# Kernel optimization log

Hardware: AMD Instinct MI355X
Metric: run time of the kernel (lower is better)

## Reference

```python
import jax, jax.numpy as jnp
import numpy as np

B_, N, C = 4096, 49, 384
H = 12
HD = C // H
NW = 64
SCALE = HD ** -0.5


def setup_inputs() -> dict:
    key = jax.random.key(0)
    k_x, k_m, k_w1, k_b1, k_w2, k_b2 = jax.random.split(key, 6)
    x = jax.random.normal(k_x, (B_, N, C), dtype=jnp.float32)
    # shifted-window style additive mask: 0 = allowed, -100 = blocked
    mask = jnp.where(jax.random.uniform(k_m, (NW, N, N)) < 0.5, 0.0, -100.0).astype(jnp.float32)
    w_qkv = jax.random.normal(k_w1, (3 * C, C), dtype=jnp.float32) * (C ** -0.5)
    b_qkv = jax.random.normal(k_b1, (3 * C,), dtype=jnp.float32) * 0.02
    w_proj = jax.random.normal(k_w2, (C, C), dtype=jnp.float32) * (C ** -0.5)
    b_proj = jax.random.normal(k_b2, (C,), dtype=jnp.float32) * 0.02
    return {"x": x, "mask": mask, "w_qkv": w_qkv, "b_qkv": b_qkv,
            "w_proj": w_proj, "b_proj": b_proj}


def reference(x, mask, w_qkv, b_qkv, w_proj, b_proj):
    # qkv projection: (B_, N, 3C)
    qkv = x @ w_qkv.T + b_qkv
    qkv = qkv.reshape(B_, N, 3, H, HD).transpose(2, 0, 3, 1, 4)  # (3, B_, H, N, HD)
    q, k, v = qkv[0], qkv[1], qkv[2]
    q = q * SCALE
    attn = jnp.einsum('bhnd,bhmd->bhnm', q, k)  # (B_, H, N, N)
    # additive shifted-window mask, per-window pattern broadcast over batch & heads
    attn = attn.reshape(B_ // NW, NW, H, N, N) + mask[None, :, None]
    attn = attn.reshape(B_, H, N, N)
    attn = jax.nn.softmax(attn, axis=-1)
    out = jnp.einsum('bhnm,bhmd->bhnd', attn, v)  # (B_, H, N, HD)
    out = out.transpose(0, 2, 1, 3).reshape(B_, N, C)
    return out @ w_proj.T + b_proj
```

## Files before the change

kernel.cpp:

```cpp
#include <hip/hip_runtime.h>
#include <cstdio>
#include <cstdint>


typedef __attribute__((ext_vector_type(8))) short bfrag8;
typedef __attribute__((ext_vector_type(4))) float facc4;
typedef __attribute__((ext_vector_type(16))) float facc16;

#define SCALE_Q 0.17677669529663687f
#define PLANE 6422528ull

__device__ __forceinline__ unsigned short f2bf(float f) {
  unsigned int x = __float_as_uint(f);
  x += 0x7fffu + ((x >> 16) & 1u);
  return (unsigned short)(x >> 16);
}

__device__ __forceinline__ void gload_lds16(const void* g, void* l) {
  __builtin_amdgcn_global_load_lds(
      (const __attribute__((address_space(1))) unsigned int*)g,
      (__attribute__((address_space(3))) unsigned int*)l,
      16, 0, 0);
}

__global__ void __launch_bounds__(256) prep_kernel(
    const float* __restrict__ wq, const float* __restrict__ wp,
    const float* __restrict__ mask,
    unsigned short* __restrict__ Bfq, unsigned short* __restrict__ Bfp,
    unsigned long long* __restrict__ bits) {
  const int blk = blockIdx.x;
  if (blk < 288) {
    const float* w = (blk < 216) ? wq : wp;
    unsigned short* Bf = (blk < 216) ? Bfq : Bfp;
    const int t = ((blk < 216) ? blk : blk - 216) * 256 + threadIdx.x;
    const int fid = t >> 6, lc = t & 63;
    const int cg = fid / 24, ksl = fid - cg * 24;
    const int col = cg * 32 + (lc & 31);
    const int k = ksl * 16 + (lc >> 5) * 8;
    const float* src = w + (size_t)col * 384 + k;
    unsigned short* dst = Bf + ((size_t)fid << 9) + (lc << 3);
#pragma unroll
    for (int j = 0; j < 8; ++j) dst[j] = f2bf(src[j]);
  } else {
    const int idx = (blk - 288) * 256 + threadIdx.x;
    const int wdw = idx >> 6, m = idx & 63;
    unsigned long long bm = 0ull;
    if (m < 49) {
      const float* mp = mask + (size_t)wdw * 2401 + (size_t)m * 49;
      for (int n = 0; n < 49; ++n)
        if (mp[n] > -50.f) bm |= (1ull << n);
    }
    bits[idx] = bm;
  }
}

#define LB32(dst, ks_)                                                         \
  {                                                                            \
    _Pragma("unroll") for (int ni = 0; ni < 3; ++ni)                           \
        dst[ni] = *(const bfrag8*)(                                            \
            Bf + ((size_t)((cg0 + ni) * 24 + (ks_)) << 9) + (lane << 3));      \
  }

#define MF32(bb, ks_)                                                          \
  {                                                                            \
    const bfrag8 af0 = *(const bfrag8*)(Ab + ((size_t)(ks_) << 10));           \
    const bfrag8 af1 = *(const bfrag8*)(Ab + ((size_t)(24 + (ks_)) << 10));    \
    _Pragma("unroll") for (int ni = 0; ni < 3; ++ni) {                         \
      acc[0][ni] = __builtin_amdgcn_mfma_f32_32x32x16_bf16(af0, bb[ni],        \
                                                           acc[0][ni], 0, 0, 0);\
      acc[1][ni] = __builtin_amdgcn_mfma_f32_32x32x16_bf16(af1, bb[ni],        \
                                                           acc[1][ni], 0, 0, 0);\
    }                                                                          \
  }

template <int NR, int MODE, int SWZ>
__global__ void __launch_bounds__(512, 1) gemm_32(
    const float* __restrict__ Af32, const unsigned short* __restrict__ Abf,
    const unsigned short* __restrict__ Bf, const float* __restrict__ bias,
    unsigned short* __restrict__ qkv, float* __restrict__ f_out) {
  __shared__ __align__(16) unsigned short Alds[128 * 384];

  int bid = blockIdx.x;
  bid = (bid & 7) * SWZ + (bid >> 3);
  const int tid = threadIdx.x;
  const int lane = tid & 63, w = tid >> 6;
  const int wr = w >> 2, wc = w & 3;
  const int l31 = lane & 31, l5 = lane >> 5;
  const size_t a_row0 = (size_t)bid * 128;

  if (MODE == 0) {
#pragma unroll
    for (int j = 0; j < 12; ++j) {
      const int fid = w + j * 8;
      const int rg = fid / 24, ksl = fid - rg * 24;
      const int row = rg * 32 + l31;
      const int k = ksl * 16 + l5 * 8;
      const float* src = Af32 + (a_row0 + row) * 384 + k;
      const float4 v0 = *(const float4*)(src);
      const float4 v1 = *(const float4*)(src + 4);
      bfrag8 h;
      h[0] = (short)f2bf(v0.x); h[1] = (short)f2bf(v0.y);
      h[2] = (short)f2bf(v0.z); h[3] = (short)f2bf(v0.w);
      h[4] = (short)f2bf(v1.x); h[5] = (short)f2bf(v1.y);
      h[6] = (short)f2bf(v1.z); h[7] = (short)f2bf(v1.w);
      *(bfrag8*)((char*)Alds + ((w << 10) + (j << 13)) + (lane << 4)) = h;
    }
  } else {
#pragma unroll
    for (int j = 0; j < 12; ++j) {
      const int fid = w + j * 8;
      const int rg = fid / 24, ksl = fid - rg * 24;
      const int row = rg * 32 + l31;
      const int k = ksl * 16 + l5 * 8;
      gload_lds16(Abf + (a_row0 + row) * 384 + k,
                  (char*)Alds + ((w << 10) + (j << 13)));
    }
  }
  __syncthreads();

  const char* Ab = (const char*)Alds + ((size_t)(wr * 48) << 10) + (lane << 4);

  for (int rnd = 0; rnd < NR; ++rnd) {
    const int cg0 = (rnd * 4 + wc) * 3;
    facc16 acc[2][3];
#pragma unroll
    for (int mi = 0; mi < 2; ++mi)
#pragma unroll
      for (int ni = 0; ni < 3; ++ni)
#pragma unroll
        for (int r = 0; r < 16; ++r) acc[mi][ni][r] = 0.f;

    bfrag8 bA[3], bB[3], bC[3];
    LB32(bA, 0);
    LB32(bB, 1);
    LB32(bC, 2);
#pragma unroll 1
    for (int ks = 0; ks < 24; ks += 3) {
      MF32(bA, ks);
      if (ks + 3 < 24) LB32(bA, ks + 3);
      MF32(bB, ks + 1);
      if (ks + 4 < 24) LB32(bB, ks + 4);
      MF32(bC, ks + 2);
      if (ks + 5 < 24) LB32(bC, ks + 5);
    }

    if (MODE == 0) {
#pragma unroll
      for (int ni = 0; ni < 3; ++ni) {
        const int j0 = (cg0 + ni) * 32;
        const int t = j0 / 384;
        const int rj = j0 - t * 384;
        const int h = rj >> 5;
        unsigned short* pl = qkv + (size_t)(t * 12 + h) * PLANE + l31;
        const float bvv = bias[j0 + l31];
        const float sc = (t == 0) ? SCALE_Q : 1.0f;
#pragma unroll
        for (int mi = 0; mi < 2; ++mi)
#pragma unroll
          for (int r = 0; r < 16; ++r) {
            const size_t m = a_row0 + wr * 64 + mi * 32 +
                             (r & 3) + 8 * (r >> 2) + 4 * l5;
            pl[m * 32] = f2bf((acc[mi][ni][r] + bvv) * sc);
          }
      }
    } else {
#pragma unroll
      for (int ni = 0; ni < 3; ++ni) {
        const int col = (cg0 + ni) * 32 + l31;
        const float bvv = bias[col];
#pragma unroll
        for (int mi = 0; mi < 2; ++mi)
#pragma unroll
          for (int r = 0; r < 16; ++r) {
            const size_t m = a_row0 + wr * 64 + mi * 32 +
                             (r & 3) + 8 * (r >> 2) + 4 * l5;
            f_out[m * 384 + col] = acc[mi][ni][r] + bvv;
          }
      }
    }
  }
}

__global__ void __launch_bounds__(64) attn_kernel(
    const unsigned short* __restrict__ QKV,
    const unsigned long long* __restrict__ mbits,
    unsigned short* __restrict__ Og) {
  __shared__ unsigned short Vt[32 * 64];
  __shared__ unsigned short Ps[64 * 64];

  const int bid = blockIdx.x;
  const int b = bid / 12, h = bid - b * 12;
  const int lane = threadIdx.x;
  const int l15 = lane & 15, l4 = lane >> 4;

  const bfrag8 z8 = {0, 0, 0, 0, 0, 0, 0, 0};
  const facc4 fz = {0.f, 0.f, 0.f, 0.f};

  const size_t wb = (size_t)b * 49 * 32;
  const unsigned short* Qp = QKV + (size_t)h * PLANE + wb;
  const unsigned short* Kp = QKV + (size_t)(12 + h) * PLANE + wb;
  const unsigned short* Vp = QKV + (size_t)(24 + h) * PLANE + wb;

#pragma unroll
  for (int i = 0; i < 4; ++i)
    *(bfrag8*)((char*)Vt + (lane + i * 64) * 16) = z8;

#pragma unroll
  for (int i = 0; i < 4; ++i) {
    const int c = lane + i * 64;
    if (c < 196) {
      const bfrag8 vv = *(const bfrag8*)(Vp + c * 8);
      const int n = c >> 2, cc = c & 3;
      const int d0 = cc * 8;
#pragma unroll
      for (int jj = 0; jj < 8; ++jj) {
        const int d = d0 + jj;
        *(unsigned short*)((char*)Vt + (((d << 7) + (n << 1)) ^ ((d & 7) << 4))) =
            (unsigned short)vv[jj];
      }
    }
  }
  __syncthreads();

  facc4 s[4][4];
  {
    bfrag8 qa[4], kf[4];
#pragma unroll
    for (int mi = 0; mi < 4; ++mi)
      qa[mi] = *(const bfrag8*)((const char*)Qp + (mi * 16 + l15) * 64 + l4 * 16);
#pragma unroll
    for (int ni = 0; ni < 4; ++ni)
      kf[ni] = *(const bfrag8*)((const char*)Kp + (ni * 16 + l15) * 64 + l4 * 16);
#pragma unroll
    for (int mi = 0; mi < 4; ++mi)
#pragma unroll
      for (int ni = 0; ni < 4; ++ni)
        s[mi][ni] = __builtin_amdgcn_mfma_f32_16x16x32_bf16(qa[mi], kf[ni], fz, 0, 0, 0);
  }

  const unsigned long long* mb = mbits + (size_t)(b & 63) * 64;
  float rinv[4][4];
#pragma unroll
  for (int mi = 0; mi < 4; ++mi)
#pragma unroll
    for (int r = 0; r < 4; ++r) {
      const int m = mi * 16 + l4 * 4 + r;
      const unsigned long long mw = mb[m];
      float mx = -1e30f;
      int ok[4];
#pragma unroll
      for (int ni = 0; ni < 4; ++ni) {
        const int n = ni * 16 + l15;
        ok[ni] = (int)((mw >> n) & 1ull);
        const float v = ok[ni] ? s[mi][ni][r] : -1e30f;
        mx = fmaxf(mx, v);
      }
      mx = fmaxf(mx, __shfl_xor(mx, 1));
      mx = fmaxf(mx, __shfl_xor(mx, 2));
      mx = fmaxf(mx, __shfl_xor(mx, 4));
      mx = fmaxf(mx, __shfl_xor(mx, 8));
      float sum = 0.f;
#pragma unroll
      for (int ni = 0; ni < 4; ++ni) {
        const float p = ok[ni] ? __expf(s[mi][ni][r] - mx) : 0.f;
        s[mi][ni][r] = p;
        sum += p;
      }
      sum += __shfl_xor(sum, 1);
      sum += __shfl_xor(sum, 2);
      sum += __shfl_xor(sum, 4);
      sum += __shfl_xor(sum, 8);
      rinv[mi][r] = 1.0f / sum;
#pragma unroll
      for (int ni = 0; ni < 4; ++ni) {
        const int n = ni * 16 + l15;
        *(unsigned short*)((char*)Ps + (((m << 7) + (n << 1)) ^ ((m & 7) << 4))) =
            f2bf(s[mi][ni][r]);
      }
    }
  __syncthreads();

  facc4 o[4][2];
#pragma unroll
  for (int mi = 0; mi < 4; ++mi)
#pragma unroll
    for (int di = 0; di < 2; ++di) o[mi][di] = fz;
#pragma unroll
  for (int kk = 0; kk < 2; ++kk) {
    bfrag8 pa[4], vb[2];
#pragma unroll
    for (int mi = 0; mi < 4; ++mi) {
      const int row = mi * 16 + l15;
      pa[mi] = *(const bfrag8*)((const char*)Ps +
                                (((row << 7) + kk * 64 + (l4 << 4)) ^ ((row & 7) << 4)));
    }
#pragma unroll
    for (int di = 0; di < 2; ++di) {
      const int row = di * 16 + l15;
      vb[di] = *(const bfrag8*)((const char*)Vt +
                                (((row << 7) + kk * 64 + (l4 << 4)) ^ ((row & 7) << 4)));
    }
#pragma unroll
    for (int mi = 0; mi < 4; ++mi)
#pragma unroll
      for (int di = 0; di < 2; ++di)
        o[mi][di] = __builtin_amdgcn_mfma_f32_16x16x32_bf16(pa[mi], vb[di], o[mi][di], 0, 0, 0);
  }

  unsigned short* op = Og + (size_t)b * 18816 + h * 32;
#pragma unroll
  for (int mi = 0; mi < 4; ++mi)
#pragma unroll
    for (int r = 0; r < 4; ++r) {
      const int m = mi * 16 + l4 * 4 + r;
      if (m < 49) {
        const float rs = rinv[mi][r];
#pragma unroll
        for (int di = 0; di < 2; ++di)
          op[(size_t)m * 384 + di * 16 + l15] = f2bf(o[mi][di][r] * rs);
      }
    }
}

extern "C" void kernel_launch(void* const* d_in, const int* in_sizes, int n_in,
                              void* d_out, int out_size, void* d_ws, size_t ws_size,
                              hipStream_t stream) {
  const float* x      = (const float*)d_in[0];
  const float* mask   = (const float*)d_in[1];
  const float* w_qkv  = (const float*)d_in[2];
  const float* b_qkv  = (const float*)d_in[3];
  const float* w_proj = (const float*)d_in[4];
  const float* b_proj = (const float*)d_in[5];
  float* out = (float*)d_out;

  const size_t E = 77070336ull;
  unsigned short* wsu   = (unsigned short*)d_ws;
  unsigned short* qkvp  = wsu;
  unsigned short* o_ws  = wsu + 3 * E;
  unsigned short* Bfq   = wsu + 4 * E;
  unsigned short* Bfp   = Bfq + 442368ull;
  unsigned long long* mb = (unsigned long long*)(Bfp + 147456ull);
  const size_t need = (4 * E + 442368ull + 147456ull) * 2ull + 4096ull * 8ull;
  if (ws_size < need) {
    fprintf(stderr, "[WindowAttention] ws too small: need=%zu have=%zu\n",
            (size_t)need, ws_size);
    return;
  }

  prep_kernel<<<304, 256, 0, stream>>>(w_qkv, w_proj, mask, Bfq, Bfp, mb);

  gemm_32<3, 0, 196><<<1568, 512, 0, stream>>>(x, nullptr, Bfq, b_qkv,
                                               qkvp, nullptr);

  attn_kernel<<<49152, 64, 0, stream>>>(qkvp, mb, o_ws);

  gemm_32<1, 1, 196><<<1568, 512, 0, stream>>>(nullptr, o_ws, Bfp, b_proj,
                                               nullptr, out);
}
```

Measured before the change: 650.5 us.

## Add weight-stationary projection GEMM and shorten QKV GEMM B prefetch depth

Adds a new output-projection GEMM kernel that stages half of the projection weight matrix (192 columns) in LDS per pass and streams the bf16 attention output rows directly from global memory into registers, instead of staging the activation tile in LDS. The QKV GEMM loses its MODE template and its B-fragment prefetch drops from three register buffers to two, which lowers register pressure but hides less load latency. The projection kernel now reloads weights twice per block and fetches the A operand from global memory inside the inner loop, so its performance depends on cache hit rates for those reads.

```diff
diff --git a/kernel.cpp b/kernel.cpp
--- a/kernel.cpp
+++ b/kernel.cpp
@@ -73,11 +73,10 @@
     }                                                                          \
   }
 
-template <int NR, int MODE, int SWZ>
+template <int NR, int SWZ>
 __global__ void __launch_bounds__(512, 1) gemm_32(
-    const float* __restrict__ Af32, const unsigned short* __restrict__ Abf,
-    const unsigned short* __restrict__ Bf, const float* __restrict__ bias,
-    unsigned short* __restrict__ qkv, float* __restrict__ f_out) {
+    const float* __restrict__ Af32, const unsigned short* __restrict__ Bf,
+    const float* __restrict__ bias, unsigned short* __restrict__ qkv) {
   __shared__ __align__(16) unsigned short Alds[128 * 384];
 
   int bid = blockIdx.x;
@@ -88,33 +87,21 @@
   const int l31 = lane & 31, l5 = lane >> 5;
   const size_t a_row0 = (size_t)bid * 128;
 
-  if (MODE == 0) {
-#pragma unroll
-    for (int j = 0; j < 12; ++j) {
-      const int fid = w + j * 8;
-      const int rg = fid / 24, ksl = fid - rg * 24;
-      const int row = rg * 32 + l31;
-      const int k = ksl * 16 + l5 * 8;
-      const float* src = Af32 + (a_row0 + row) * 384 + k;
-      const float4 v0 = *(const float4*)(src);
-      const float4 v1 = *(const float4*)(src + 4);
-      bfrag8 h;
-      h[0] = (short)f2bf(v0.x); h[1] = (short)f2bf(v0.y);
-      h[2] = (short)f2bf(v0.z); h[3] = (short)f2bf(v0.w);
-      h[4] = (short)f2bf(v1.x); h[5] = (short)f2bf(v1.y);
-      h[6] = (short)f2bf(v1.z); h[7] = (short)f2bf(v1.w);
-      *(bfrag8*)((char*)Alds + ((w << 10) + (j << 13)) + (lane << 4)) = h;
-    }
-  } else {
-#pragma unroll
-    for (int j = 0; j < 12; ++j) {
-      const int fid = w + j * 8;
-      const int rg = fid / 24, ksl = fid - rg * 24;
-      const int row = rg * 32 + l31;
-      const int k = ksl * 16 + l5 * 8;
-      gload_lds16(Abf + (a_row0 + row) * 384 + k,
-                  (char*)Alds + ((w << 10) + (j << 13)));
-    }
+#pragma unroll
+  for (int j = 0; j < 12; ++j) {
+    const int fid = w + j * 8;
+    const int rg = fid / 24, ksl = fid - rg * 24;
+    const int row = rg * 32 + l31;
+    const int k = ksl * 16 + l5 * 8;
+    const float* src = Af32 + (a_row0 + row) * 384 + k;
+    const float4 v0 = *(const float4*)(src);
+    const float4 v1 = *(const float4*)(src + 4);
+    bfrag8 h;
+    h[0] = (short)f2bf(v0.x); h[1] = (short)f2bf(v0.y);
+    h[2] = (short)f2bf(v0.z); h[3] = (short)f2bf(v0.w);
+    h[4] = (short)f2bf(v1.x); h[5] = (short)f2bf(v1.y);
+    h[6] = (short)f2bf(v1.z); h[7] = (short)f2bf(v1.w);
+    *(bfrag8*)((char*)Alds + ((w << 10) + (j << 13)) + (lane << 4)) = h;
   }
   __syncthreads();
 
@@ -130,54 +117,99 @@
 #pragma unroll
         for (int r = 0; r < 16; ++r) acc[mi][ni][r] = 0.f;
 
-    bfrag8 bA[3], bB[3], bC[3];
+    bfrag8 bA[3], bB[3];
     LB32(bA, 0);
     LB32(bB, 1);
-    LB32(bC, 2);
 #pragma unroll 1
-    for (int ks = 0; ks < 24; ks += 3) {
+    for (int ks = 0; ks < 24; ks += 2) {
       MF32(bA, ks);
-      if (ks + 3 < 24) LB32(bA, ks + 3);
+      if (ks + 2 < 24) LB32(bA, ks + 2);
       MF32(bB, ks + 1);
-      if (ks + 4 < 24) LB32(bB, ks + 4);
-      MF32(bC, ks + 2);
-      if (ks + 5 < 24) LB32(bC, ks + 5);
-    }
-
-    if (MODE == 0) {
-#pragma unroll
-      for (int ni = 0; ni < 3; ++ni) {
-        const int j0 = (cg0 + ni) * 32;
-        const int t = j0 / 384;
-        const int rj = j0 - t * 384;
-        const int h = rj >> 5;
-        unsigned short* pl = qkv + (size_t)(t * 12 + h) * PLANE + l31;
-        const float bvv = bias[j0 + l31];
-        const float sc = (t == 0) ? SCALE_Q : 1.0f;
-#pragma unroll
-        for (int mi = 0; mi < 2; ++mi)
-#pragma unroll
-          for (int r = 0; r < 16; ++r) {
-            const size_t m = a_row0 + wr * 64 + mi * 32 +
-                             (r & 3) + 8 * (r >> 2) + 4 * l5;
-            pl[m * 32] = f2bf((acc[mi][ni][r] + bvv) * sc);
-          }
-      }
-    } else {
-#pragma unroll
-      for (int ni = 0; ni < 3; ++ni) {
-        const int col = (cg0 + ni) * 32 + l31;
-        const float bvv = bias[col];
-#pragma unroll
-        for (int mi = 0; mi < 2; ++mi)
-#pragma unroll
-          for (int r = 0; r < 16; ++r) {
-            const size_t m = a_row0 + wr * 64 + mi * 32 +
-                             (r & 3) + 8 * (r >> 2) + 4 * l5;
-            f_out[m * 384 + col] = acc[mi][ni][r] + bvv;
-          }
-      }
-    }
+      if (ks + 3 < 24) LB32(bB, ks + 3);
+    }
+
+#pragma unroll
+    for (int ni = 0; ni < 3; ++ni) {
+      const int j0 = (cg0 + ni) * 32;
+      const int t = j0 / 384;
+      const int rj = j0 - t * 384;
+      const int h = rj >> 5;
+      unsigned short* pl = qkv + (size_t)(t * 12 + h) * PLANE + l31;
+      const float bvv = bias[j0 + l31];
+      const float sc = (t == 0) ? SCALE_Q : 1.0f;
+#pragma unroll
+      for (int mi = 0; mi < 2; ++mi)
+#pragma unroll
+        for (int r = 0; r < 16; ++r) {
+          const size_t m = a_row0 + wr * 64 + mi * 32 +
+                           (r & 3) + 8 * (r >> 2) + 4 * l5;
+          pl[m * 32] = f2bf((acc[mi][ni][r] + bvv) * sc);
+        }
+    }
+  }
+}
+
+template <int SWZ>
+__global__ void __launch_bounds__(512, 1) gemm_wp(
+    const unsigned short* __restrict__ O, const unsigned short* __restrict__ Bfp,
+    const float* __restrict__ bias, float* __restrict__ out) {
+  __shared__ __align__(16) unsigned short Wlds[144 * 512];
+
+  int bid = blockIdx.x;
+  bid = (bid & 7) * SWZ + (bid >> 3);
+  const int tid = threadIdx.x;
+  const int lane = tid & 63, w = tid >> 6;
+  const int wr = w >> 1, wc = w & 1;
+  const int l31 = lane & 31, l5 = lane >> 5;
+  const size_t a_row0 = (size_t)bid * 128;
+
+  const unsigned short* Orow = O + (a_row0 + wr * 32 + l31) * 384 + l5 * 8;
+  const char* Wb = (const char*)Wlds + ((size_t)(wc * 72) << 10) + (lane << 4);
+
+  for (int nh = 0; nh < 2; ++nh) {
+#pragma unroll
+    for (int j = 0; j < 18; ++j) {
+      const int fidl = w + j * 8;
+      gload_lds16(Bfp + ((size_t)(nh * 144 + fidl) << 9) + (lane << 3),
+                  (char*)Wlds + ((w << 10) + (j << 13)));
+    }
+    __syncthreads();
+
+    facc16 acc[3];
+#pragma unroll
+    for (int ni = 0; ni < 3; ++ni)
+#pragma unroll
+      for (int r = 0; r < 16; ++r) acc[ni][r] = 0.f;
+
+    bfrag8 oA = *(const bfrag8*)(Orow);
+    bfrag8 oB = *(const bfrag8*)(Orow + 16);
+#pragma unroll 1
+    for (int ks = 0; ks < 24; ks += 2) {
+#pragma unroll
+      for (int ni = 0; ni < 3; ++ni)
+        acc[ni] = __builtin_amdgcn_mfma_f32_32x32x16_bf16(
+            oA, *(const bfrag8*)(Wb + ((size_t)(ni * 24 + ks) << 10)),
+            acc[ni], 0, 0, 0);
+      if (ks + 2 < 24) oA = *(const bfrag8*)(Orow + (ks + 2) * 16);
+#pragma unroll
+      for (int ni = 0; ni < 3; ++ni)
+        acc[ni] = __builtin_amdgcn_mfma_f32_32x32x16_bf16(
+            oB, *(const bfrag8*)(Wb + ((size_t)(ni * 24 + ks + 1) << 10)),
+            acc[ni], 0, 0, 0);
+      if (ks + 3 < 24) oB = *(const bfrag8*)(Orow + (ks + 3) * 16);
+    }
+
+#pragma unroll
+    for (int ni = 0; ni < 3; ++ni) {
+      const int col = nh * 192 + (wc * 3 + ni) * 32 + l31;
+      const float bvv = bias[col];
+#pragma unroll
+      for (int r = 0; r < 16; ++r) {
+        const size_t m = a_row0 + wr * 32 + (r & 3) + 8 * (r >> 2) + 4 * l5;
+        out[m * 384 + col] = acc[ni][r] + bvv;
+      }
+    }
+    __syncthreads();
   }
 }
 
@@ -349,11 +381,9 @@
 
   prep_kernel<<<304, 256, 0, stream>>>(w_qkv, w_proj, mask, Bfq, Bfp, mb);
 
-  gemm_32<3, 0, 196><<<1568, 512, 0, stream>>>(x, nullptr, Bfq, b_qkv,
-                                               qkvp, nullptr);
+  gemm_32<3, 196><<<1568, 512, 0, stream>>>(x, Bfq, b_qkv, qkvp);
 
   attn_kernel<<<49152, 64, 0, stream>>>(qkvp, mb, o_ws);
 
-  gemm_32<1, 1, 196><<<1568, 512, 0, stream>>>(nullptr, o_ws, Bfp, b_proj,
-                                               nullptr, out);
-}
+  gemm_wp<196><<<1568, 512, 0, stream>>>(o_ws, Bfp, b_proj, out);
+}
```

After: 680.7 us. +4.6%, slower.
